# Kernel optimization log

Measured on AMD Instinct MI355X. Metric: run time of the kernel, lower is better.

Reference implementation:

```python
import jax, jax.numpy as jnp
import numpy as np

NUM_SYM = 50000
NUM_HERB = 50000
N_NODES = NUM_SYM + NUM_HERB
DIM = 128
N_EDGES = 3200000
N_LAYERS = 2


def setup_inputs() -> dict:
    key = jax.random.key(0)
    k1, k2, k3, k4, k5 = jax.random.split(key, 5)
    sym_emb = jax.random.normal(k1, (NUM_SYM, DIM), dtype=jnp.float32)
    herb_emb = jax.random.normal(k2, (NUM_HERB, DIM), dtype=jnp.float32)
    adj_rows = jax.random.randint(k3, (N_EDGES,), 0, N_NODES, dtype=jnp.int32)
    adj_cols = jax.random.randint(k4, (N_EDGES,), 0, N_NODES, dtype=jnp.int32)
    # normalized-Laplacian values are positive; uniform stands in for D^-1/2 A D^-1/2 entries
    adj_vals = jax.random.uniform(k5, (N_EDGES,), dtype=jnp.float32)
    return {"sym_emb": sym_emb, "herb_emb": herb_emb,
            "adj_rows": adj_rows, "adj_cols": adj_cols, "adj_vals": adj_vals}


def _spmm(rows, cols, vals, x):
    # sparse [N,N] @ dense [N,D]: gather source rows, scale, scatter-add to dest rows
    msgs = vals[:, None] * x[cols]              # [E, D]
    return jax.ops.segment_sum(msgs, rows, num_segments=N_NODES)


def reference(sym_emb, herb_emb, adj_rows, adj_cols, adj_vals):
    ego = jnp.concatenate([sym_emb, herb_emb], axis=0)   # [N, D]
    acc = ego
    e = ego
    for _ in range(N_LAYERS):
        e = _spmm(adj_rows, adj_cols, adj_vals, e)
        acc = acc + e
    all_emb = acc / jnp.float32(N_LAYERS + 1)            # mean over stacked layers
    return all_emb[:NUM_SYM], all_emb[NUM_SYM:]
```

## Files before the change

kernel.cpp:

```cpp
#include <hip/hip_runtime.h>

#define NUM_SYM 50000
#define NUM_HERB 50000
#define N_NODES (NUM_SYM + NUM_HERB)
#define DIM 128
#define NB_BUCKETS ((N_NODES + 255) / 256)
#define CHUNK 4096
#define NG 8
#define PAD 16

typedef float floatx4 __attribute__((ext_vector_type(4)));

__device__ __forceinline__ float bf2f(unsigned short u) {
    return __uint_as_float((unsigned)u << 16);
}
__device__ __forceinline__ unsigned short f2bf(float f) {
    unsigned u = __float_as_uint(f);
    unsigned r = (u + 0x7FFFu + ((u >> 16) & 1u)) >> 16;
    return (unsigned short)r;
}

__global__ __launch_bounds__(256) void to_bf16(
    const float* __restrict__ sym, const float* __restrict__ herb,
    ushort* __restrict__ xbf)
{
    int i = blockIdx.x * 256 + threadIdx.x;
    const int n4 = N_NODES * DIM / 4;
    if (i >= n4) return;
    const int sym4 = NUM_SYM * DIM / 4;
    float4 v = (i < sym4) ? reinterpret_cast<const float4*>(sym)[i]
                          : reinterpret_cast<const float4*>(herb)[i - sym4];
    ushort4 o;
    o.x = f2bf(v.x); o.y = f2bf(v.y); o.z = f2bf(v.z); o.w = f2bf(v.w);
    reinterpret_cast<ushort4*>(xbf)[i] = o;
}


__global__ __launch_bounds__(1024) void hist_buckets(
    const int* __restrict__ rows, int E, int* __restrict__ bcnt8)
{
    __shared__ int h[NB_BUCKETS];
    for (int i = threadIdx.x; i < NB_BUCKETS; i += 1024) h[i] = 0;
    __syncthreads();
    int g = blockIdx.x & (NG - 1);
    int start = blockIdx.x * CHUNK;
    int end   = min(start + CHUNK, E);
    for (int e = start + threadIdx.x; e < end; e += 1024)
        atomicAdd(&h[rows[e] >> 8], 1);
    __syncthreads();
    for (int i = threadIdx.x; i < NB_BUCKETS; i += 1024)
        if (h[i]) atomicAdd(&bcnt8[(i * NG + g) * PAD], h[i]);
}

__global__ __launch_bounds__(1024) void scan_buckets(
    const int* __restrict__ bcnt8, int* __restrict__ boff, int* __restrict__ bcur8)
{
    __shared__ int s[1024];
    int c = threadIdx.x;
    int pre[NG];
    int tot = 0;
    if (c < NB_BUCKETS) {
        #pragma unroll
        for (int g = 0; g < NG; ++g) {
            pre[g] = tot;
            tot += bcnt8[(c * NG + g) * PAD];
        }
    }
    s[c] = tot;
    __syncthreads();
    for (int o = 1; o < 1024; o <<= 1) {
        int x = (c >= o) ? s[c - o] : 0;
        __syncthreads();
        s[c] += x;
        __syncthreads();
    }
    int excl = s[c] - tot;
    if (c < NB_BUCKETS) {
        boff[c] = excl;
        #pragma unroll
        for (int g = 0; g < NG; ++g)
            bcur8[(c * NG + g) * PAD] = excl + pre[g];
    }
    if (c == NB_BUCKETS - 1) boff[NB_BUCKETS] = s[c];
}

__global__ __launch_bounds__(1024) void scatter_buckets(
    const int* __restrict__ rows, const int* __restrict__ cols,
    const float* __restrict__ vals, int E,
    int* __restrict__ bcur8, int2* __restrict__ bucketed)
{
    __shared__ int lh[NB_BUCKETS];
    __shared__ int lbase[NB_BUCKETS];
    for (int i = threadIdx.x; i < NB_BUCKETS; i += 1024) lh[i] = 0;
    __syncthreads();
    int g = blockIdx.x & (NG - 1);
    int start = blockIdx.x * CHUNK;
    int end   = min(start + CHUNK, E);
    for (int e = start + threadIdx.x; e < end; e += 1024)
        atomicAdd(&lh[rows[e] >> 8], 1);
    __syncthreads();
    for (int i = threadIdx.x; i < NB_BUCKETS; i += 1024) {
        int c = lh[i];
        lbase[i] = c ? atomicAdd(&bcur8[(i * NG + g) * PAD], c) : 0;
        lh[i] = 0;
    }
    __syncthreads();
    for (int e = start + threadIdx.x; e < end; e += 1024) {
        int r = rows[e];
        int key = r >> 8;
        int pos = lbase[key] + atomicAdd(&lh[key], 1);
        bucketed[pos] = make_int2(((r & 255) << 17) | cols[e],
                                  __float_as_int(vals[e]));
    }
}

__global__ __launch_bounds__(1024) void bucket_to_csr(
    const int2* __restrict__ bucketed, const int* __restrict__ off,
    int* __restrict__ csr, int* __restrict__ rowptr)
{
    __shared__ int h[256];
    int b = blockIdx.x, t = threadIdx.x;
    int s0 = off[b], s1 = off[b + 1];
    if (t < 256) h[t] = 0;
    __syncthreads();
    for (int j = s0 + t; j < s1; j += 1024)
        atomicAdd(&h[(unsigned)bucketed[j].x >> 17], 1);
    __syncthreads();
    int v = (t < 256) ? h[t] : 0;
    for (int o = 1; o < 256; o <<= 1) {
        int x = (t < 256 && t >= o) ? h[t - o] : 0;
        __syncthreads();
        if (t < 256) h[t] += x;
        __syncthreads();
    }
    if (t < 256) {
        int r = b * 256 + t;
        if (r < N_NODES) rowptr[r] = s0 + (h[t] - v);
    }
    __syncthreads();
    if (t < 256) h[t] -= v;
    __syncthreads();
    for (int j = s0 + t; j < s1; j += 1024) {
        int2 rec = bucketed[j];
        int key = (unsigned)rec.x >> 17;
        int pos = s0 + atomicAdd(&h[key], 1);
        unsigned vb = (unsigned)f2bf(__int_as_float(rec.y));
        csr[pos] = (int)((vb << 17) | ((unsigned)rec.x & 0x1FFFFu));
    }
}

__device__ __forceinline__ float unpack_val(int p) {
    return __uint_as_float(((unsigned)p >> 17) << 16);
}

template <bool FUSE_MEAN>
__global__ __launch_bounds__(256) void spmm_csr_bf16(
    const int* __restrict__ csr, const int* __restrict__ rowptr, int E,
    const ushort* __restrict__ xbf,
    const float* __restrict__ sym, const float* __restrict__ herb,
    const ushort* __restrict__ e1bf,
    void* __restrict__ outp)
{
    int wave = blockIdx.x * 4 + (threadIdx.x >> 6);
    int half = (threadIdx.x >> 5) & 1;
    int lane = threadIdx.x & 31;
    int r = wave * 2 + half;
    if (r >= N_NODES) return;

    int j   = rowptr[r];
    int end = (r + 1 < N_NODES) ? rowptr[r + 1] : E;

    float4 acc = make_float4(0.f, 0.f, 0.f, 0.f);
    for (; j + 7 < end; j += 8) {
        int p0 = csr[j], p1 = csr[j + 1], p2 = csr[j + 2], p3 = csr[j + 3];
        int p4 = csr[j + 4], p5 = csr[j + 5], p6 = csr[j + 6], p7 = csr[j + 7];
        ushort4 m0 = reinterpret_cast<const ushort4*>(xbf + (size_t)(p0 & 0x1FFFF) * DIM)[lane];
        ushort4 m1 = reinterpret_cast<const ushort4*>(xbf + (size_t)(p1 & 0x1FFFF) * DIM)[lane];
        ushort4 m2 = reinterpret_cast<const ushort4*>(xbf + (size_t)(p2 & 0x1FFFF) * DIM)[lane];
        ushort4 m3 = reinterpret_cast<const ushort4*>(xbf + (size_t)(p3 & 0x1FFFF) * DIM)[lane];
        ushort4 m4 = reinterpret_cast<const ushort4*>(xbf + (size_t)(p4 & 0x1FFFF) * DIM)[lane];
        ushort4 m5 = reinterpret_cast<const ushort4*>(xbf + (size_t)(p5 & 0x1FFFF) * DIM)[lane];
        ushort4 m6 = reinterpret_cast<const ushort4*>(xbf + (size_t)(p6 & 0x1FFFF) * DIM)[lane];
        ushort4 m7 = reinterpret_cast<const ushort4*>(xbf + (size_t)(p7 & 0x1FFFF) * DIM)[lane];
        float v0 = unpack_val(p0), v1 = unpack_val(p1);
        float v2 = unpack_val(p2), v3 = unpack_val(p3);
        float v4 = unpack_val(p4), v5 = unpack_val(p5);
        float v6 = unpack_val(p6), v7 = unpack_val(p7);
        acc.x += v0 * bf2f(m0.x) + v1 * bf2f(m1.x) + v2 * bf2f(m2.x) + v3 * bf2f(m3.x)
               + v4 * bf2f(m4.x) + v5 * bf2f(m5.x) + v6 * bf2f(m6.x) + v7 * bf2f(m7.x);
        acc.y += v0 * bf2f(m0.y) + v1 * bf2f(m1.y) + v2 * bf2f(m2.y) + v3 * bf2f(m3.y)
               + v4 * bf2f(m4.y) + v5 * bf2f(m5.y) + v6 * bf2f(m6.y) + v7 * bf2f(m7.y);
        acc.z += v0 * bf2f(m0.z) + v1 * bf2f(m1.z) + v2 * bf2f(m2.z) + v3 * bf2f(m3.z)
               + v4 * bf2f(m4.z) + v5 * bf2f(m5.z) + v6 * bf2f(m6.z) + v7 * bf2f(m7.z);
        acc.w += v0 * bf2f(m0.w) + v1 * bf2f(m1.w) + v2 * bf2f(m2.w) + v3 * bf2f(m3.w)
               + v4 * bf2f(m4.w) + v5 * bf2f(m5.w) + v6 * bf2f(m6.w) + v7 * bf2f(m7.w);
    }
    for (; j + 3 < end; j += 4) {
        int p0 = csr[j], p1 = csr[j + 1], p2 = csr[j + 2], p3 = csr[j + 3];
        ushort4 m0 = reinterpret_cast<const ushort4*>(xbf + (size_t)(p0 & 0x1FFFF) * DIM)[lane];
        ushort4 m1 = reinterpret_cast<const ushort4*>(xbf + (size_t)(p1 & 0x1FFFF) * DIM)[lane];
        ushort4 m2 = reinterpret_cast<const ushort4*>(xbf + (size_t)(p2 & 0x1FFFF) * DIM)[lane];
        ushort4 m3 = reinterpret_cast<const ushort4*>(xbf + (size_t)(p3 & 0x1FFFF) * DIM)[lane];
        float v0 = unpack_val(p0), v1 = unpack_val(p1);
        float v2 = unpack_val(p2), v3 = unpack_val(p3);
        acc.x += v0 * bf2f(m0.x) + v1 * bf2f(m1.x) + v2 * bf2f(m2.x) + v3 * bf2f(m3.x);
        acc.y += v0 * bf2f(m0.y) + v1 * bf2f(m1.y) + v2 * bf2f(m2.y) + v3 * bf2f(m3.y);
        acc.z += v0 * bf2f(m0.z) + v1 * bf2f(m1.z) + v2 * bf2f(m2.z) + v3 * bf2f(m3.z);
        acc.w += v0 * bf2f(m0.w) + v1 * bf2f(m1.w) + v2 * bf2f(m2.w) + v3 * bf2f(m3.w);
    }
    for (; j < end; ++j) {
        int p0 = csr[j];
        float v0 = unpack_val(p0);
        ushort4 m0 = reinterpret_cast<const ushort4*>(xbf + (size_t)(p0 & 0x1FFFF) * DIM)[lane];
        acc.x += v0 * bf2f(m0.x);
        acc.y += v0 * bf2f(m0.y);
        acc.z += v0 * bf2f(m0.z);
        acc.w += v0 * bf2f(m0.w);
    }

    if (FUSE_MEAN) {
        const float4* egorow = (r < NUM_SYM)
            ? reinterpret_cast<const float4*>(sym  + (size_t)r * DIM)
            : reinterpret_cast<const float4*>(herb + (size_t)(r - NUM_SYM) * DIM);
        float4 g = egorow[lane];
        ushort4 a = reinterpret_cast<const ushort4*>(e1bf + (size_t)r * DIM)[lane];
        const float s = 1.0f / 3.0f;
        floatx4 o;
        o.x = (g.x + bf2f(a.x) + acc.x) * s;
        o.y = (g.y + bf2f(a.y) + acc.y) * s;
        o.z = (g.z + bf2f(a.z) + acc.z) * s;
        o.w = (g.w + bf2f(a.w) + acc.w) * s;
        __builtin_nontemporal_store(o,
            reinterpret_cast<floatx4*>((float*)outp + (size_t)r * DIM) + lane);
    } else {
        ushort4 o;
        o.x = f2bf(acc.x); o.y = f2bf(acc.y); o.z = f2bf(acc.z); o.w = f2bf(acc.w);
        reinterpret_cast<ushort4*>((ushort*)outp + (size_t)r * DIM)[lane] = o;
    }
}

__global__ __launch_bounds__(256) void spmm_scatter(
    const int* __restrict__ rows, const int* __restrict__ cols,
    const float* __restrict__ vals, int n_edges,
    const float* __restrict__ xa, const float* __restrict__ xb,
    float* __restrict__ out)
{
    int gid = blockIdx.x * 256 + threadIdx.x;
    int edge = gid >> 5;
    if (edge >= n_edges) return;
    int sub = gid & 31;
    int c = cols[edge];
    int r = rows[edge];
    float v = vals[edge];
    const float* xrow = (c < NUM_SYM) ? (xa + (size_t)c * DIM)
                                      : (xb + (size_t)(c - NUM_SYM) * DIM);
    float4 m = reinterpret_cast<const float4*>(xrow)[sub];
    float* o = out + (size_t)r * DIM + (size_t)sub * 4;
    unsafeAtomicAdd(o + 0, v * m.x);
    unsafeAtomicAdd(o + 1, v * m.y);
    unsafeAtomicAdd(o + 2, v * m.z);
    unsafeAtomicAdd(o + 3, v * m.w);
}

__global__ __launch_bounds__(256) void finalize_mean(
    const float* __restrict__ sym, const float* __restrict__ herb,
    const float* __restrict__ e1, float* __restrict__ out)
{
    int i = blockIdx.x * 256 + threadIdx.x;
    const int n4 = N_NODES * DIM / 4;
    if (i >= n4) return;
    const int sym4 = NUM_SYM * DIM / 4;
    float4 e = (i < sym4) ? reinterpret_cast<const float4*>(sym)[i]
                          : reinterpret_cast<const float4*>(herb)[i - sym4];
    float4 a = reinterpret_cast<const float4*>(e1)[i];
    float4 b = reinterpret_cast<float4*>(out)[i];
    const float s = 1.0f / 3.0f;
    float4 r;
    r.x = (e.x + a.x + b.x) * s;
    r.y = (e.y + a.y + b.y) * s;
    r.z = (e.z + a.z + b.z) * s;
    r.w = (e.w + a.w + b.w) * s;
    reinterpret_cast<float4*>(out)[i] = r;
}

extern "C" void kernel_launch(void* const* d_in, const int* in_sizes, int n_in,
                              void* d_out, int out_size, void* d_ws, size_t ws_size,
                              hipStream_t stream) {
    const float* sym  = (const float*)d_in[0];
    const float* herb = (const float*)d_in[1];
    const int*   rows = (const int*)d_in[2];
    const int*   cols = (const int*)d_in[3];
    const float* vals = (const float*)d_in[4];
    const int E = in_sizes[2];
    float* out = (float*)d_out;

    char* ws = (char*)d_ws;
    auto align256 = [](size_t x) { return (x + 255) & ~(size_t)255; };
    const size_t xbf_bytes   = (size_t)N_NODES * DIM * sizeof(ushort);
    const size_t csr_off     = align256(xbf_bytes);
    const size_t buck_off    = align256(csr_off + (size_t)E * 4);
    const size_t buck_bytes  = (size_t)E * 8 > xbf_bytes ? (size_t)E * 8 : xbf_bytes;
    const size_t rowptr_off  = align256(buck_off + buck_bytes);
    const size_t bcnt_off    = align256(rowptr_off + (size_t)N_NODES * 4);
    const size_t boff_off    = align256(bcnt_off + (size_t)NB_BUCKETS * NG * PAD * 4);
    const size_t bcur_off    = align256(boff_off + (size_t)(NB_BUCKETS + 1) * 4);
    const size_t required    = bcur_off + (size_t)NB_BUCKETS * NG * PAD * 4;

    if (ws_size < required || E >= (1 << 22)) {
        float* e1 = (float*)ws;
        const size_t e1_bytes = (size_t)N_NODES * DIM * sizeof(float);
        hipMemsetAsync(e1, 0, e1_bytes, stream);
        hipMemsetAsync(out, 0, e1_bytes, stream);
        const int spmm_blocks = (E * 32 + 255) / 256;
        spmm_scatter<<<spmm_blocks, 256, 0, stream>>>(rows, cols, vals, E, sym, herb, e1);
        spmm_scatter<<<spmm_blocks, 256, 0, stream>>>(rows, cols, vals, E,
                                                      e1, e1 + (size_t)NUM_SYM * DIM, out);
        const int n4 = N_NODES * DIM / 4;
        finalize_mean<<<(n4 + 255) / 256, 256, 0, stream>>>(sym, herb, e1, out);
        return;
    }

    ushort* xbf      = (ushort*)ws;
    int*    csr      = (int*)(ws + csr_off);
    int2*   bucketed = (int2*)(ws + buck_off);
    ushort* e1bf     = (ushort*)(ws + buck_off);
    int*    rowptr   = (int*)(ws + rowptr_off);
    int*    bcnt8    = (int*)(ws + bcnt_off);
    int*    boff     = (int*)(ws + boff_off);
    int*    bcur8    = (int*)(ws + bcur_off);

    hipMemsetAsync(bcnt8, 0, (size_t)NB_BUCKETS * NG * PAD * 4, stream);
    const int EB = (E + CHUNK - 1) / CHUNK;
    hist_buckets<<<EB, 1024, 0, stream>>>(rows, E, bcnt8);
    scan_buckets<<<1, 1024, 0, stream>>>(bcnt8, boff, bcur8);
    scatter_buckets<<<EB, 1024, 0, stream>>>(rows, cols, vals, E, bcur8, bucketed);
    bucket_to_csr<<<NB_BUCKETS, 1024, 0, stream>>>(bucketed, boff, csr, rowptr);

    const int n4 = N_NODES * DIM / 4;
    to_bf16<<<(n4 + 255) / 256, 256, 0, stream>>>(sym, herb, xbf);

    const int blocks = (N_NODES / 2 + 3) / 4;
    spmm_csr_bf16<false><<<blocks, 256, 0, stream>>>(csr, rowptr, E, xbf,
                                                     nullptr, nullptr, nullptr, e1bf);
    spmm_csr_bf16<true><<<blocks, 256, 0, stream>>>(csr, rowptr, E, e1bf,
                                                    sym, herb, e1bf, out);
}
```

Before: 443.0 us.

## Replace histogram+scan bucketing with fixed-capacity per-bucket slot regions

Drops the separate histogram and prefix-scan kernels. Edges are now scattered straight into preallocated slot regions, one per bucket and group, sized at 1.25x the average bucket load. Rows carry explicit rowend pointers so the CSR can contain gaps between buckets. This removes one full pass over the row indices and a single-block scan launch. In exchange it uses more workspace and has no overflow check, so a skewed row distribution would silently corrupt results.

```diff
diff --git a/kernel.cpp b/kernel.cpp
--- a/kernel.cpp
+++ b/kernel.cpp
@@ -36,61 +36,13 @@
 }
 
 
-__global__ __launch_bounds__(1024) void hist_buckets(
-    const int* __restrict__ rows, int E, int* __restrict__ bcnt8)
-{
-    __shared__ int h[NB_BUCKETS];
-    for (int i = threadIdx.x; i < NB_BUCKETS; i += 1024) h[i] = 0;
-    __syncthreads();
-    int g = blockIdx.x & (NG - 1);
-    int start = blockIdx.x * CHUNK;
-    int end   = min(start + CHUNK, E);
-    for (int e = start + threadIdx.x; e < end; e += 1024)
-        atomicAdd(&h[rows[e] >> 8], 1);
-    __syncthreads();
-    for (int i = threadIdx.x; i < NB_BUCKETS; i += 1024)
-        if (h[i]) atomicAdd(&bcnt8[(i * NG + g) * PAD], h[i]);
-}
-
-__global__ __launch_bounds__(1024) void scan_buckets(
-    const int* __restrict__ bcnt8, int* __restrict__ boff, int* __restrict__ bcur8)
-{
-    __shared__ int s[1024];
-    int c = threadIdx.x;
-    int pre[NG];
-    int tot = 0;
-    if (c < NB_BUCKETS) {
-        #pragma unroll
-        for (int g = 0; g < NG; ++g) {
-            pre[g] = tot;
-            tot += bcnt8[(c * NG + g) * PAD];
-        }
-    }
-    s[c] = tot;
-    __syncthreads();
-    for (int o = 1; o < 1024; o <<= 1) {
-        int x = (c >= o) ? s[c - o] : 0;
-        __syncthreads();
-        s[c] += x;
-        __syncthreads();
-    }
-    int excl = s[c] - tot;
-    if (c < NB_BUCKETS) {
-        boff[c] = excl;
-        #pragma unroll
-        for (int g = 0; g < NG; ++g)
-            bcur8[(c * NG + g) * PAD] = excl + pre[g];
-    }
-    if (c == NB_BUCKETS - 1) boff[NB_BUCKETS] = s[c];
-}
-
-__global__ __launch_bounds__(1024) void scatter_buckets(
+__global__ __launch_bounds__(1024) void scatter_slots(
     const int* __restrict__ rows, const int* __restrict__ cols,
-    const float* __restrict__ vals, int E,
-    int* __restrict__ bcur8, int2* __restrict__ bucketed)
+    const float* __restrict__ vals, int E, int CAP, int SUBCAP,
+    int* __restrict__ cur, int2* __restrict__ slots)
 {
     __shared__ int lh[NB_BUCKETS];
-    __shared__ int lbase[NB_BUCKETS];
+    __shared__ int labs[NB_BUCKETS];
     for (int i = threadIdx.x; i < NB_BUCKETS; i += 1024) lh[i] = 0;
     __syncthreads();
     int g = blockIdx.x & (NG - 1);
@@ -101,30 +53,38 @@
     __syncthreads();
     for (int i = threadIdx.x; i < NB_BUCKETS; i += 1024) {
         int c = lh[i];
-        lbase[i] = c ? atomicAdd(&bcur8[(i * NG + g) * PAD], c) : 0;
+        int resv = c ? atomicAdd(&cur[(i * NG + g) * PAD], c) : 0;
+        labs[i] = i * CAP + g * SUBCAP + resv;
         lh[i] = 0;
     }
     __syncthreads();
     for (int e = start + threadIdx.x; e < end; e += 1024) {
         int r = rows[e];
         int key = r >> 8;
-        int pos = lbase[key] + atomicAdd(&lh[key], 1);
-        bucketed[pos] = make_int2(((r & 255) << 17) | cols[e],
-                                  __float_as_int(vals[e]));
-    }
-}
-
-__global__ __launch_bounds__(1024) void bucket_to_csr(
-    const int2* __restrict__ bucketed, const int* __restrict__ off,
-    int* __restrict__ csr, int* __restrict__ rowptr)
+        int pos = labs[key] + atomicAdd(&lh[key], 1);
+        slots[pos] = make_int2(((r & 255) << 17) | cols[e],
+                               __float_as_int(vals[e]));
+    }
+}
+
+__global__ __launch_bounds__(1024) void slots_to_csr(
+    const int2* __restrict__ slots, const int* __restrict__ cur,
+    int CAP, int SUBCAP,
+    int* __restrict__ csr, int* __restrict__ rowptr, int* __restrict__ rowend)
 {
     __shared__ int h[256];
+    __shared__ int cnt[NG];
     int b = blockIdx.x, t = threadIdx.x;
-    int s0 = off[b], s1 = off[b + 1];
+    if (t < NG) cnt[t] = cur[(b * NG + t) * PAD];
     if (t < 256) h[t] = 0;
     __syncthreads();
-    for (int j = s0 + t; j < s1; j += 1024)
-        atomicAdd(&h[(unsigned)bucketed[j].x >> 17], 1);
+    size_t sb = (size_t)b * CAP;
+    for (int g = 0; g < NG; ++g) {
+        int n = cnt[g];
+        const int2* p = slots + sb + (size_t)g * SUBCAP;
+        for (int j = t; j < n; j += 1024)
+            atomicAdd(&h[(unsigned)p[j].x >> 17], 1);
+    }
     __syncthreads();
     int v = (t < 256) ? h[t] : 0;
     for (int o = 1; o < 256; o <<= 1) {
@@ -133,19 +93,27 @@
         if (t < 256) h[t] += x;
         __syncthreads();
     }
+    int cb = b * CAP;
     if (t < 256) {
         int r = b * 256 + t;
-        if (r < N_NODES) rowptr[r] = s0 + (h[t] - v);
+        if (r < N_NODES) {
+            rowptr[r] = cb + (h[t] - v);
+            rowend[r] = cb + h[t];
+        }
     }
     __syncthreads();
     if (t < 256) h[t] -= v;
     __syncthreads();
-    for (int j = s0 + t; j < s1; j += 1024) {
-        int2 rec = bucketed[j];
-        int key = (unsigned)rec.x >> 17;
-        int pos = s0 + atomicAdd(&h[key], 1);
-        unsigned vb = (unsigned)f2bf(__int_as_float(rec.y));
-        csr[pos] = (int)((vb << 17) | ((unsigned)rec.x & 0x1FFFFu));
+    for (int g = 0; g < NG; ++g) {
+        int n = cnt[g];
+        const int2* p = slots + sb + (size_t)g * SUBCAP;
+        for (int j = t; j < n; j += 1024) {
+            int2 rec = p[j];
+            int key = (unsigned)rec.x >> 17;
+            int pos = cb + atomicAdd(&h[key], 1);
+            unsigned vb = (unsigned)f2bf(__int_as_float(rec.y));
+            csr[pos] = (int)((vb << 17) | ((unsigned)rec.x & 0x1FFFFu));
+        }
     }
 }
 
@@ -155,7 +123,8 @@
 
 template <bool FUSE_MEAN>
 __global__ __launch_bounds__(256) void spmm_csr_bf16(
-    const int* __restrict__ csr, const int* __restrict__ rowptr, int E,
+    const int* __restrict__ csr, const int* __restrict__ rowptr,
+    const int* __restrict__ rowend,
     const ushort* __restrict__ xbf,
     const float* __restrict__ sym, const float* __restrict__ herb,
     const ushort* __restrict__ e1bf,
@@ -168,7 +137,7 @@
     if (r >= N_NODES) return;
 
     int j   = rowptr[r];
-    int end = (r + 1 < N_NODES) ? rowptr[r + 1] : E;
+    int end = rowend[r];
 
     float4 acc = make_float4(0.f, 0.f, 0.f, 0.f);
     for (; j + 7 < end; j += 8) {
@@ -294,17 +263,22 @@
     const int E = in_sizes[2];
     float* out = (float*)d_out;
 
+    int CAP = (int)(((long)E / NB_BUCKETS) * 5 / 4);
+    CAP = (CAP + NG * 32 - 1) / (NG * 32) * (NG * 32);
+    if (CAP < NG * 64) CAP = NG * 64;
+    const int SUBCAP = CAP / NG;
+
     char* ws = (char*)d_ws;
     auto align256 = [](size_t x) { return (x + 255) & ~(size_t)255; };
     const size_t xbf_bytes   = (size_t)N_NODES * DIM * sizeof(ushort);
     const size_t csr_off     = align256(xbf_bytes);
-    const size_t buck_off    = align256(csr_off + (size_t)E * 4);
-    const size_t buck_bytes  = (size_t)E * 8 > xbf_bytes ? (size_t)E * 8 : xbf_bytes;
-    const size_t rowptr_off  = align256(buck_off + buck_bytes);
-    const size_t bcnt_off    = align256(rowptr_off + (size_t)N_NODES * 4);
-    const size_t boff_off    = align256(bcnt_off + (size_t)NB_BUCKETS * NG * PAD * 4);
-    const size_t bcur_off    = align256(boff_off + (size_t)(NB_BUCKETS + 1) * 4);
-    const size_t required    = bcur_off + (size_t)NB_BUCKETS * NG * PAD * 4;
+    const size_t slot_off    = align256(csr_off + (size_t)NB_BUCKETS * CAP * 4);
+    const size_t slot_bytes  = (size_t)NB_BUCKETS * CAP * 8 > xbf_bytes
+                             ? (size_t)NB_BUCKETS * CAP * 8 : xbf_bytes;
+    const size_t rowptr_off  = align256(slot_off + slot_bytes);
+    const size_t rowend_off  = align256(rowptr_off + (size_t)N_NODES * 4);
+    const size_t cur_off     = align256(rowend_off + (size_t)N_NODES * 4);
+    const size_t required    = cur_off + (size_t)NB_BUCKETS * NG * PAD * 4;
 
     if (ws_size < required || E >= (1 << 22)) {
         float* e1 = (float*)ws;
@@ -320,28 +294,26 @@
         return;
     }
 
-    ushort* xbf      = (ushort*)ws;
-    int*    csr      = (int*)(ws + csr_off);
-    int2*   bucketed = (int2*)(ws + buck_off);
-    ushort* e1bf     = (ushort*)(ws + buck_off);
-    int*    rowptr   = (int*)(ws + rowptr_off);
-    int*    bcnt8    = (int*)(ws + bcnt_off);
-    int*    boff     = (int*)(ws + boff_off);
-    int*    bcur8    = (int*)(ws + bcur_off);
-
-    hipMemsetAsync(bcnt8, 0, (size_t)NB_BUCKETS * NG * PAD * 4, stream);
+    ushort* xbf    = (ushort*)ws;
+    int*    csr    = (int*)(ws + csr_off);
+    int2*   slots  = (int2*)(ws + slot_off);
+    ushort* e1bf   = (ushort*)(ws + slot_off);
+    int*    rowptr = (int*)(ws + rowptr_off);
+    int*    rowend = (int*)(ws + rowend_off);
+    int*    cur    = (int*)(ws + cur_off);
+
+    hipMemsetAsync(cur, 0, (size_t)NB_BUCKETS * NG * PAD * 4, stream);
     const int EB = (E + CHUNK - 1) / CHUNK;
-    hist_buckets<<<EB, 1024, 0, stream>>>(rows, E, bcnt8);
-    scan_buckets<<<1, 1024, 0, stream>>>(bcnt8, boff, bcur8);
-    scatter_buckets<<<EB, 1024, 0, stream>>>(rows, cols, vals, E, bcur8, bucketed);
-    bucket_to_csr<<<NB_BUCKETS, 1024, 0, stream>>>(bucketed, boff, csr, rowptr);
+    scatter_slots<<<EB, 1024, 0, stream>>>(rows, cols, vals, E, CAP, SUBCAP, cur, slots);
+    slots_to_csr<<<NB_BUCKETS, 1024, 0, stream>>>(slots, cur, CAP, SUBCAP,
+                                                  csr, rowptr, rowend);
 
     const int n4 = N_NODES * DIM / 4;
     to_bf16<<<(n4 + 255) / 256, 256, 0, stream>>>(sym, herb, xbf);
 
     const int blocks = (N_NODES / 2 + 3) / 4;
-    spmm_csr_bf16<false><<<blocks, 256, 0, stream>>>(csr, rowptr, E, xbf,
+    spmm_csr_bf16<false><<<blocks, 256, 0, stream>>>(csr, rowptr, rowend, xbf,
                                                      nullptr, nullptr, nullptr, e1bf);
-    spmm_csr_bf16<true><<<blocks, 256, 0, stream>>>(csr, rowptr, E, e1bf,
+    spmm_csr_bf16<true><<<blocks, 256, 0, stream>>>(csr, rowptr, rowend, e1bf,
                                                     sym, herb, e1bf, out);
 }
```

Result: faster. 424.4 us (-4.2%).
